# Optimization experiments

Measured on AMD Instinct MI355X. Metric: run time of the kernel, lower is better.

## Reference

```python
import jax, jax.numpy as jnp
import numpy as np

N = 50000          # nodes
E = 800000         # random edges (self-loops added in reference, per PyG default)
B = 64             # graphs in batch
IN_DIM = 773
HID = 256
OUT = 128
H1, D1 = 4, 64     # heads, head_dim layer 1 (256 = 4*64)
H2, D2 = 4, 32     # heads, head_dim layer 2 (128 = 4*32)
NEG_SLOPE = 0.2


def setup_inputs() -> dict:
    key = jax.random.key(0)
    ks = jax.random.split(key, 20)
    s = 0.02
    x = jax.random.normal(ks[0], (N, IN_DIM), dtype=jnp.float32)
    edge_index = jax.random.randint(ks[1], (2, E), 0, N, dtype=jnp.int32)
    batch = jnp.sort(jax.random.randint(ks[2], (N,), 0, B, dtype=jnp.int32))
    return {
        "x": x,
        "edge_index": edge_index,
        "batch": batch,
        "W_in": jax.random.normal(ks[3], (IN_DIM, HID), jnp.float32) * s,
        "b_in": jnp.zeros((HID,), jnp.float32),
        "W1": jax.random.normal(ks[4], (HID, H1 * D1), jnp.float32) * s,
        "att_src1": jax.random.normal(ks[5], (H1, D1), jnp.float32) * s,
        "att_dst1": jax.random.normal(ks[6], (H1, D1), jnp.float32) * s,
        "b1": jnp.zeros((H1 * D1,), jnp.float32),
        "W2": jax.random.normal(ks[7], (HID, H2 * D2), jnp.float32) * s,
        "att_src2": jax.random.normal(ks[8], (H2, D2), jnp.float32) * s,
        "att_dst2": jax.random.normal(ks[9], (H2, D2), jnp.float32) * s,
        "b2": jnp.zeros((H2 * D2,), jnp.float32),
        "W_cls": jax.random.normal(ks[10], (OUT, 2), jnp.float32) * s,
        "b_cls": jnp.zeros((2,), jnp.float32),
        "W_conf": jax.random.normal(ks[11], (OUT, 1), jnp.float32) * s,
        "b_conf": jnp.zeros((1,), jnp.float32),
    }


def _gat_layer(h, src, dst, W, att_src, att_dst, bias, heads, dim):
    # h: (N, F_in). PyG GATConv, concat=True, eval mode (dropout off).
    hW = (h @ W).reshape(N, heads, dim)                    # (N, H, D)
    a_src = jnp.einsum("nhd,hd->nh", hW, att_src)          # (N, H)
    a_dst = jnp.einsum("nhd,hd->nh", hW, att_dst)
    e = a_src[src] + a_dst[dst]                            # (E', H)
    e = jax.nn.leaky_relu(e, NEG_SLOPE)
    # segment softmax over incoming edges of each dst node
    m = jax.ops.segment_max(e, dst, num_segments=N)        # (N, H)
    ex = jnp.exp(e - m[dst])
    z = jax.ops.segment_sum(ex, dst, num_segments=N)       # (N, H)
    alpha = ex / (z[dst] + 1e-16)                          # (E', H)
    msg = hW[src] * alpha[:, :, None]                      # (E', H, D)
    out = jax.ops.segment_sum(msg, dst, num_segments=N)    # (N, H, D)
    return out.reshape(N, heads * dim) + bias


def reference(x, edge_index, batch, W_in, b_in,
              W1, att_src1, att_dst1, b1,
              W2, att_src2, att_dst2, b2,
              W_cls, b_cls, W_conf, b_conf):
    loops = jnp.arange(N, dtype=edge_index.dtype)
    src = jnp.concatenate([edge_index[0], loops])
    dst = jnp.concatenate([edge_index[1], loops])

    h = jax.nn.relu(x @ W_in + b_in)                       # (N, 256)
    h = jax.nn.relu(_gat_layer(h, src, dst, W1, att_src1, att_dst1, b1, H1, D1))
    h = _gat_layer(h, src, dst, W2, att_src2, att_dst2, b2, H2, D2)
    h = jax.nn.relu(h)                                     # (N, 128)

    # global mean pool over graphs
    sums = jax.ops.segment_sum(h, batch, num_segments=B)   # (B, 128)
    cnts = jax.ops.segment_sum(jnp.ones((N,), h.dtype), batch, num_segments=B)
    graph_emb = sums / jnp.maximum(cnts, 1.0)[:, None]

    class_logits = graph_emb @ W_cls + b_cls               # (B, 2)
    confidence = jax.nn.sigmoid(graph_emb @ W_conf + b_conf)  # (B, 1)
    return class_logits, confidence
```

## Files before the change

kernel.cpp:

```cpp
#include <hip/hip_runtime.h>
#include <math.h>

#define NN 50000
#define NE 800000
#define NB 64
#define IND 773
#define MPAD 50048
#define SCAN_B 196

typedef __attribute__((ext_vector_type(8))) short short8_t;
typedef __attribute__((ext_vector_type(4))) float f32x4;

__device__ __forceinline__ float lrelu(float x) { return x > 0.f ? x : 0.2f * x; }
__device__ __forceinline__ short f2b(float f) {
    unsigned u = __float_as_uint(f);
    unsigned r = (u + 0x7fffu + ((u >> 16) & 1u)) >> 16;
    return (short)r;
}
__device__ __forceinline__ float b2f(short s) {
    return __uint_as_float(((unsigned)(unsigned short)s) << 16);
}

#define GLOAD16(g, l) __builtin_amdgcn_global_load_lds(                         \
    (const __attribute__((address_space(1))) void*)(g),                         \
    (__attribute__((address_space(3))) void*)(l), 16, 0, 0)

__global__ __launch_bounds__(512) void gemm_a(const float* __restrict__ X,
                                              const short* __restrict__ Bt,
                                              const float* __restrict__ bias,
                                              short* __restrict__ C) {
    const int K = 800, N = 256;
    __shared__ short As[128 * 32];
    __shared__ short Bs[256 * 32];
    const int t = threadIdx.x;
    const int w = t >> 6, l = t & 63;
    const int l15 = l & 15, lh = l >> 4;
    const int bm = blockIdx.x * 128;
    const int wr = (w >> 2) * 64, wc = (w & 3) * 64;

    const short* bG = Bt + (size_t)(t >> 2) * K + (t & 3) * 8;
    short* bLu = Bs + w * 512;

    f32x4 acc[4][4];
#pragma unroll
    for (int i = 0; i < 4; ++i)
#pragma unroll
        for (int j = 0; j < 4; ++j) acc[i][j] = (f32x4){0.f, 0.f, 0.f, 0.f};

    for (int k0 = 0; k0 < K; k0 += 32) {
        __syncthreads();
        GLOAD16(bG + k0, bLu);
        GLOAD16(bG + (size_t)128 * K + k0, bLu + 128 * 32);
#pragma unroll
        for (int i = 0; i < 4; ++i) {
            int fid = i * 512 + t;
            int row = fid >> 4;
            int cp = fid & 15;
            int gm = bm + row;
            int gk = k0 + cp * 2;
            const float* xp = X + (size_t)gm * IND + gk;
            bool rowok = (gm < NN);
            float v0 = (rowok && gk < IND) ? xp[0] : 0.f;
            float v1 = (rowok && gk + 1 < IND) ? xp[1] : 0.f;
            unsigned pk = ((unsigned)(unsigned short)f2b(v0)) |
                          (((unsigned)(unsigned short)f2b(v1)) << 16);
            *(unsigned*)&As[row * 32 + cp * 2] = pk;
        }
        __syncthreads();
        short8_t af[4], bfr[4];
#pragma unroll
        for (int mi = 0; mi < 4; ++mi)
            af[mi] = *(const short8_t*)&As[(wr + mi * 16 + l15) * 32 + lh * 8];
#pragma unroll
        for (int ni = 0; ni < 4; ++ni)
            bfr[ni] = *(const short8_t*)&Bs[(wc + ni * 16 + l15) * 32 + lh * 8];
#pragma unroll
        for (int mi = 0; mi < 4; ++mi)
#pragma unroll
            for (int ni = 0; ni < 4; ++ni)
                acc[mi][ni] = __builtin_amdgcn_mfma_f32_16x16x32_bf16(af[mi], bfr[ni], acc[mi][ni], 0, 0, 0);
    }
#pragma unroll
    for (int mi = 0; mi < 4; ++mi) {
#pragma unroll
        for (int r = 0; r < 4; ++r) {
            int grow = bm + wr + mi * 16 + lh * 4 + r;
            if (grow >= NN) continue;
#pragma unroll
            for (int ni = 0; ni < 4; ++ni) {
                int gcol = wc + ni * 16 + l15;
                float v = fmaxf(acc[mi][ni][r] + bias[gcol], 0.f);
                C[(size_t)grow * N + gcol] = f2b(v);
            }
        }
    }
}

__global__ __launch_bounds__(512) void gemm_b(const short* __restrict__ A,
                                              const short* __restrict__ Bt,
                                              const float* __restrict__ att_s,
                                              const float* __restrict__ att_d,
                                              short* __restrict__ C,
                                              float* __restrict__ a_s,
                                              float* __restrict__ a_d) {
    const int K = 256, N = 256;
    __shared__ short As[128 * 32];
    __shared__ short Bs[256 * 32];
    const int t = threadIdx.x;
    const int w = t >> 6, l = t & 63;
    const int l15 = l & 15, lh = l >> 4;
    const int bm = blockIdx.x * 128;
    const int wr = (w >> 2) * 64, wc = (w & 3) * 64;

    const short* aG = A + (size_t)(bm + (t >> 2)) * K + (t & 3) * 8;
    const short* bG = Bt + (size_t)(t >> 2) * K + (t & 3) * 8;
    short* aLu = As + w * 512;
    short* bLu = Bs + w * 512;

    f32x4 acc[4][4];
#pragma unroll
    for (int i = 0; i < 4; ++i)
#pragma unroll
        for (int j = 0; j < 4; ++j) acc[i][j] = (f32x4){0.f, 0.f, 0.f, 0.f};

    for (int k0 = 0; k0 < K; k0 += 32) {
        __syncthreads();
        GLOAD16(aG + k0, aLu);
        GLOAD16(bG + k0, bLu);
        GLOAD16(bG + (size_t)128 * K + k0, bLu + 128 * 32);
        __syncthreads();
        short8_t af[4], bfr[4];
#pragma unroll
        for (int mi = 0; mi < 4; ++mi)
            af[mi] = *(const short8_t*)&As[(wr + mi * 16 + l15) * 32 + lh * 8];
#pragma unroll
        for (int ni = 0; ni < 4; ++ni)
            bfr[ni] = *(const short8_t*)&Bs[(wc + ni * 16 + l15) * 32 + lh * 8];
#pragma unroll
        for (int mi = 0; mi < 4; ++mi)
#pragma unroll
            for (int ni = 0; ni < 4; ++ni)
                acc[mi][ni] = __builtin_amdgcn_mfma_f32_16x16x32_bf16(af[mi], bfr[ni], acc[mi][ni], 0, 0, 0);
    }
    const int head = wc >> 6;
    float sa[4], sd[4];
#pragma unroll
    for (int ni = 0; ni < 4; ++ni) {
        sa[ni] = att_s[head * 64 + ni * 16 + l15];
        sd[ni] = att_d[head * 64 + ni * 16 + l15];
    }
#pragma unroll
    for (int mi = 0; mi < 4; ++mi) {
#pragma unroll
        for (int r = 0; r < 4; ++r) {
            int grow = bm + wr + mi * 16 + lh * 4 + r;
            float s = acc[mi][0][r] * sa[0] + acc[mi][1][r] * sa[1] +
                      acc[mi][2][r] * sa[2] + acc[mi][3][r] * sa[3];
            float d = acc[mi][0][r] * sd[0] + acc[mi][1][r] * sd[1] +
                      acc[mi][2][r] * sd[2] + acc[mi][3][r] * sd[3];
#pragma unroll
            for (int off = 1; off < 16; off <<= 1) {
                s += __shfl_xor(s, off);
                d += __shfl_xor(d, off);
            }
            if (grow < NN) {
                if (l15 == 0) { a_s[grow * 4 + head] = s; a_d[grow * 4 + head] = d; }
#pragma unroll
                for (int ni = 0; ni < 4; ++ni)
                    C[(size_t)grow * N + wc + ni * 16 + l15] = f2b(acc[mi][ni][r]);
            }
        }
    }
}

__global__ __launch_bounds__(256) void gemm_c(const short* __restrict__ A,
                                              const short* __restrict__ Bt,
                                              const float* __restrict__ att_s,
                                              const float* __restrict__ att_d,
                                              short* __restrict__ C,
                                              float* __restrict__ a_s,
                                              float* __restrict__ a_d) {
    const int K = 256, N = 128;
    __shared__ short As[128 * 32];
    __shared__ short Bs[128 * 32];
    const int t = threadIdx.x;
    const int w = t >> 6, l = t & 63;
    const int l15 = l & 15, lh = l >> 4;
    const int bm = blockIdx.x * 128;
    const int wr = (w >> 1) * 64, wc = (w & 1) * 64;

    const short* aG = A + (size_t)(bm + w * 32 + (l >> 2)) * K + (l & 3) * 8;
    const short* bG = Bt + (size_t)(w * 32 + (l >> 2)) * K + (l & 3) * 8;
    short* aL = As + (w * 32) * 32;
    short* bL = Bs + (w * 32) * 32;

    f32x4 acc[4][4];
#pragma unroll
    for (int i = 0; i < 4; ++i)
#pragma unroll
        for (int j = 0; j < 4; ++j) acc[i][j] = (f32x4){0.f, 0.f, 0.f, 0.f};

    for (int k0 = 0; k0 < K; k0 += 32) {
        __syncthreads();
        GLOAD16(aG + k0, aL);
        GLOAD16(aG + (size_t)16 * K + k0, aL + 16 * 32);
        GLOAD16(bG + k0, bL);
        GLOAD16(bG + (size_t)16 * K + k0, bL + 16 * 32);
        __syncthreads();
        short8_t af[4], bfr[4];
#pragma unroll
        for (int mi = 0; mi < 4; ++mi)
            af[mi] = *(const short8_t*)&As[(wr + mi * 16 + l15) * 32 + lh * 8];
#pragma unroll
        for (int ni = 0; ni < 4; ++ni)
            bfr[ni] = *(const short8_t*)&Bs[(wc + ni * 16 + l15) * 32 + lh * 8];
#pragma unroll
        for (int mi = 0; mi < 4; ++mi)
#pragma unroll
            for (int ni = 0; ni < 4; ++ni)
                acc[mi][ni] = __builtin_amdgcn_mfma_f32_16x16x32_bf16(af[mi], bfr[ni], acc[mi][ni], 0, 0, 0);
    }
    const int h0 = wc >> 5;
    float sa[4], sd[4];
#pragma unroll
    for (int ni = 0; ni < 4; ++ni) {
        int idx = (h0 + (ni >> 1)) * 32 + (ni & 1) * 16 + l15;
        sa[ni] = att_s[idx];
        sd[ni] = att_d[idx];
    }
#pragma unroll
    for (int mi = 0; mi < 4; ++mi) {
#pragma unroll
        for (int r = 0; r < 4; ++r) {
            int grow = bm + wr + mi * 16 + lh * 4 + r;
            float s0 = acc[mi][0][r] * sa[0] + acc[mi][1][r] * sa[1];
            float s1 = acc[mi][2][r] * sa[2] + acc[mi][3][r] * sa[3];
            float d0 = acc[mi][0][r] * sd[0] + acc[mi][1][r] * sd[1];
            float d1 = acc[mi][2][r] * sd[2] + acc[mi][3][r] * sd[3];
#pragma unroll
            for (int off = 1; off < 16; off <<= 1) {
                s0 += __shfl_xor(s0, off); s1 += __shfl_xor(s1, off);
                d0 += __shfl_xor(d0, off); d1 += __shfl_xor(d1, off);
            }
            if (grow < NN) {
                if (l15 == 0) {
                    a_s[grow * 4 + h0] = s0; a_s[grow * 4 + h0 + 1] = s1;
                    a_d[grow * 4 + h0] = d0; a_d[grow * 4 + h0 + 1] = d1;
                }
#pragma unroll
                for (int ni = 0; ni < 4; ++ni)
                    C[(size_t)grow * N + wc + ni * 16 + l15] = f2b(acc[mi][ni][r]);
            }
        }
    }
}

__global__ __launch_bounds__(256) void k_wt_t(const float* __restrict__ W,
                                              short* __restrict__ Wt,
                                              int K, int N, int Kp) {
    __shared__ short tile[32][33];
    int kb = blockIdx.x * 32, nb = blockIdx.y * 32;
    int tx = threadIdx.x & 31, ty = threadIdx.x >> 5;
#pragma unroll
    for (int r = 0; r < 32; r += 8) {
        int k = kb + ty + r;
        tile[ty + r][tx] = (k < K) ? f2b(W[(size_t)k * N + nb + tx]) : (short)0;
    }
    __syncthreads();
#pragma unroll
    for (int r = 0; r < 32; r += 8) {
        int n = nb + ty + r, k = kb + tx;
        Wt[(size_t)n * Kp + k] = tile[tx][ty + r];
    }
}

__global__ __launch_bounds__(256) void k_zero(int* __restrict__ p, int n) {
    int i = blockIdx.x * 256 + threadIdx.x;
    if (i < n) p[i] = 0;
}

__global__ void k_hist(const int* __restrict__ ei, int* __restrict__ deg) {
    int e = blockIdx.x * 256 + threadIdx.x;
    if (e >= NE) return;
    atomicAdd(&deg[ei[NE + e]], 1);
}

__global__ __launch_bounds__(256) void k_bsum(const int* __restrict__ deg,
                                              int* __restrict__ bsum) {
    int i = blockIdx.x * 256 + threadIdx.x;
    int v = (i < NN) ? deg[i] : 0;
#pragma unroll
    for (int off = 32; off; off >>= 1) v += __shfl_down(v, off);
    __shared__ int ws[4];
    if ((threadIdx.x & 63) == 0) ws[threadIdx.x >> 6] = v;
    __syncthreads();
    if (threadIdx.x == 0) bsum[blockIdx.x] = ws[0] + ws[1] + ws[2] + ws[3];
}

__global__ __launch_bounds__(256) void k_bscan(const int* __restrict__ bsum,
                                               int* __restrict__ boff) {
    int t = threadIdx.x;
    int orig = (t < SCAN_B) ? bsum[t] : 0;
    int v = orig;
    int lane = t & 63, wid = t >> 6;
#pragma unroll
    for (int off = 1; off < 64; off <<= 1) {
        int u = __shfl_up(v, off);
        if (lane >= off) v += u;
    }
    __shared__ int ws[4];
    if (lane == 63) ws[wid] = v;
    __syncthreads();
    int add = 0;
    for (int wq = 0; wq < wid; ++wq) add += ws[wq];
    if (t < SCAN_B) boff[t] = v + add - orig;
}

__global__ __launch_bounds__(256) void k_scan3(const int* __restrict__ deg,
                                               const int* __restrict__ boff,
                                               int* __restrict__ rowp,
                                               int* __restrict__ cursor) {
    int b = blockIdx.x;
    int i = b * 256 + threadIdx.x;
    int d = (i < NN) ? deg[i] : 0;
    int v = d;
    int lane = threadIdx.x & 63, wid = threadIdx.x >> 6;
#pragma unroll
    for (int off = 1; off < 64; off <<= 1) {
        int u = __shfl_up(v, off);
        if (lane >= off) v += u;
    }
    __shared__ int ws[4];
    if (lane == 63) ws[wid] = v;
    __syncthreads();
    int add = boff[b];
    for (int wq = 0; wq < wid; ++wq) add += ws[wq];
    int excl = add + v - d;
    if (i < NN) { rowp[i] = excl; cursor[i] = excl; }
    if (i == NN - 1) rowp[NN] = excl + d;
}

__global__ void k_scatter(const int* __restrict__ ei, int* __restrict__ cursor,
                          int* __restrict__ colidx) {
    int e = blockIdx.x * 256 + threadIdx.x;
    if (e >= NE) return;
    int s = ei[e], d = ei[NE + e];
    int pos = atomicAdd(&cursor[d], 1);
    colidx[pos] = s;
}

template<int HD>
__global__ __launch_bounds__(256) void gat_agg(const short* __restrict__ hW,
                                               const float* __restrict__ a_s,
                                               const float* __restrict__ a_d,
                                               const int* __restrict__ row_ptr,
                                               const int* __restrict__ colidx,
                                               const float* __restrict__ bias,
                                               short* __restrict__ outp) {
    const int CPL = HD / 64;
    int node = blockIdx.x * 4 + (threadIdx.x >> 6);
    int lane = threadIdx.x & 63;
    if (node >= NN) return;
    int h = lane >> 4;
    int start = row_ptr[node], end = row_ptr[node + 1];
    float adst = a_d[node * 4 + h];
    float eself = lrelu(a_s[node * 4 + h] + adst);

    float z = 1.f;
    float acc[CPL];
    {
        const short* row = hW + (size_t)node * HD + lane * CPL;
        if (CPL == 4) { short4 q = *(const short4*)row; acc[0]=b2f(q.x); acc[1]=b2f(q.y); acc[2]=b2f(q.z); acc[3]=b2f(q.w); }
        else          { short2 q = *(const short2*)row; acc[0]=b2f(q.x); acc[1]=b2f(q.y); }
    }
    for (int e = start; e < end; e += 8) {
        int sidx[8];
        float xs[8], ex[8];
#pragma unroll
        for (int q = 0; q < 8; ++q) {
            int ee = e + q;
            sidx[q] = colidx[ee < end ? ee : end - 1];
        }
#pragma unroll
        for (int q = 0; q < 8; ++q) xs[q] = a_s[sidx[q] * 4 + h];
        float v[8][CPL];
        if (CPL == 4) {
#pragma unroll
            for (int q = 0; q < 8; ++q) {
                short4 qq = *(const short4*)(hW + (size_t)sidx[q] * HD + lane * 4);
                v[q][0]=b2f(qq.x); v[q][1]=b2f(qq.y); v[q][2]=b2f(qq.z); v[q][3]=b2f(qq.w);
            }
        } else {
#pragma unroll
            for (int q = 0; q < 8; ++q) {
                short2 qq = *(const short2*)(hW + (size_t)sidx[q] * HD + lane * 2);
                v[q][0]=b2f(qq.x); v[q][1]=b2f(qq.y);
            }
        }
#pragma unroll
        for (int q = 0; q < 8; ++q) {
            float w = __expf(lrelu(xs[q] + adst) - eself);
            ex[q] = (e + q < end) ? w : 0.f;
        }
#pragma unroll
        for (int q = 0; q < 8; ++q) z += ex[q];
#pragma unroll
        for (int j = 0; j < CPL; ++j) {
            float a = 0.f;
#pragma unroll
            for (int q = 0; q < 8; ++q) a += ex[q] * v[q][j];
            acc[j] += a;
        }
    }
    float inv = 1.f / z;
    short* orow = outp + (size_t)node * HD + lane * CPL;
#pragma unroll
    for (int j = 0; j < CPL; ++j)
        orow[j] = f2b(fmaxf(acc[j] * inv + bias[lane * CPL + j], 0.f));
}

__global__ __launch_bounds__(512) void pool_head(const short* __restrict__ h2,
                                                 const int* __restrict__ batch,
                                                 const float* __restrict__ W_cls,
                                                 const float* __restrict__ b_cls,
                                                 const float* __restrict__ W_conf,
                                                 const float* __restrict__ b_conf,
                                                 float* __restrict__ out) {
    int b = blockIdx.x;
    int t = threadIdx.x & 127;
    int g = threadIdx.x >> 7;
    int lo = 0, hi = NN;
    while (lo < hi) { int mid = (lo + hi) >> 1; if (batch[mid] < b) lo = mid + 1; else hi = mid; }
    int start = lo;
    lo = 0; hi = NN;
    while (lo < hi) { int mid = (lo + hi) >> 1; if (batch[mid] < b + 1) lo = mid + 1; else hi = mid; }
    int end = lo;

    float acc = 0.f;
    for (int n = start + g; n < end; n += 4) acc += b2f(h2[(size_t)n * 128 + t]);
    __shared__ float se[4][128];
    se[g][t] = acc;
    __syncthreads();
    if (g == 0) {
        float emb = (se[0][t] + se[1][t] + se[2][t] + se[3][t]) /
                    fmaxf((float)(end - start), 1.f);
        se[0][t] = emb;
    }
    __syncthreads();
    if (threadIdx.x == 0) {
        float v = b_cls[0];
        for (int c = 0; c < 128; ++c) v += se[0][c] * W_cls[c * 2 + 0];
        out[b * 2 + 0] = v;
    } else if (threadIdx.x == 1) {
        float v = b_cls[1];
        for (int c = 0; c < 128; ++c) v += se[0][c] * W_cls[c * 2 + 1];
        out[b * 2 + 1] = v;
    } else if (threadIdx.x == 2) {
        float v = b_conf[0];
        for (int c = 0; c < 128; ++c) v += se[0][c] * W_conf[c];
        out[128 + b] = 1.f / (1.f + expf(-v));
    }
}

extern "C" void kernel_launch(void* const* d_in, const int* in_sizes, int n_in,
                              void* d_out, int out_size, void* d_ws, size_t ws_size,
                              hipStream_t stream) {
    const float* x        = (const float*)d_in[0];
    const int*   ei       = (const int*)d_in[1];
    const int*   batch    = (const int*)d_in[2];
    const float* W_in     = (const float*)d_in[3];
    const float* b_in     = (const float*)d_in[4];
    const float* W1       = (const float*)d_in[5];
    const float* att_src1 = (const float*)d_in[6];
    const float* att_dst1 = (const float*)d_in[7];
    const float* b1       = (const float*)d_in[8];
    const float* W2       = (const float*)d_in[9];
    const float* att_src2 = (const float*)d_in[10];
    const float* att_dst2 = (const float*)d_in[11];
    const float* b2       = (const float*)d_in[12];
    const float* W_cls    = (const float*)d_in[13];
    const float* b_cls    = (const float*)d_in[14];
    const float* W_conf   = (const float*)d_in[15];
    const float* b_conf   = (const float*)d_in[16];
    float* out = (float*)d_out;

    char* ws = (char*)d_ws;
    short* h0  = (short*)(ws + 0);
    short* hW1 = (short*)(ws + 25624576);
    short* h1  = (short*)(ws + 51249152);
    short* hW2 = (short*)(ws + 76873728);
    short* h2  = (short*)(ws + 89686016);
    size_t base = 102498304;
    short* Wt_in = (short*)(ws + base);
    short* Wt1   = (short*)(ws + base + 409600);
    short* Wt2   = (short*)(ws + base + 540672);
    float* a_s1  = (float*)(ws + base + 606208);
    float* a_d1  = (float*)(ws + base + 1406208);
    int*   deg    = (int*)(ws + base + 2206208);
    int*   rowp   = (int*)(ws + base + 2406208);
    int*   cursor = (int*)(ws + base + 2606272);
    int*   colidx = (int*)(ws + base + 2806272);
    int*   bsum   = (int*)(ws + base + 6006272);
    int*   boff   = (int*)(ws + base + 6007296);

    k_wt_t<<<dim3(25, 8), 256, 0, stream>>>(W_in, Wt_in, IND, 256, 800);
    k_wt_t<<<dim3(8, 8), 256, 0, stream>>>(W1, Wt1, 256, 256, 256);
    k_wt_t<<<dim3(8, 4), 256, 0, stream>>>(W2, Wt2, 256, 128, 256);

    k_zero<<<SCAN_B, 256, 0, stream>>>(deg, NN);
    k_hist<<<NE / 256, 256, 0, stream>>>(ei, deg);
    k_bsum<<<SCAN_B, 256, 0, stream>>>(deg, bsum);
    k_bscan<<<1, 256, 0, stream>>>(bsum, boff);
    k_scan3<<<SCAN_B, 256, 0, stream>>>(deg, boff, rowp, cursor);
    k_scatter<<<NE / 256, 256, 0, stream>>>(ei, cursor, colidx);

    gemm_a<<<391, 512, 0, stream>>>(x, Wt_in, b_in, h0);
    gemm_b<<<391, 512, 0, stream>>>(h0, Wt1, att_src1, att_dst1, hW1, a_s1, a_d1);
    gat_agg<256><<<12500, 256, 0, stream>>>(hW1, a_s1, a_d1, rowp, colidx, b1, h1);
    gemm_c<<<391, 256, 0, stream>>>(h1, Wt2, att_src2, att_dst2, hW2, a_s1, a_d1);
    gat_agg<128><<<12500, 256, 0, stream>>>(hW2, a_s1, a_d1, rowp, colidx, b2, h2);
    pool_head<<<NB, 512, 0, stream>>>(h2, batch, W_cls, b_cls, W_conf, b_conf, out);
}
```

Measured before the change: 409.3 us.

## Double-buffer input GEMM with register prefetch and split layer-1 GEMM over columns

The first GEMM now keeps two LDS buffers. It prefetches the next X tile into registers, using vectorized float4 loads converted to bf16, while MFMAs run on the current tile, so each k-step needs one barrier instead of two. The layer-1 GEMM switches from 512-thread blocks covering all 256 columns to 256-thread blocks over a 2D grid of 128-column tiles. That doubles the block count, which should improve occupancy and wave balance. The costs are extra LDS use, more register pressure in gemm_a, and A tiles being re-read once per column tile in gemm_b.

```diff
diff --git a/kernel.cpp b/kernel.cpp
--- a/kernel.cpp
+++ b/kernel.cpp
@@ -29,17 +29,19 @@
                                               const short* __restrict__ Bt,
                                               const float* __restrict__ bias,
                                               short* __restrict__ C) {
-    const int K = 800, N = 256;
-    __shared__ short As[128 * 32];
-    __shared__ short Bs[256 * 32];
+    const int K = 800, N = 256, NT = 25;
+    __shared__ short As[2][128 * 32];
+    __shared__ short Bs[2][256 * 32];
     const int t = threadIdx.x;
     const int w = t >> 6, l = t & 63;
     const int l15 = l & 15, lh = l >> 4;
     const int bm = blockIdx.x * 128;
     const int wr = (w >> 2) * 64, wc = (w & 3) * 64;
-
+    const int arow = t >> 2, acb = (t & 3) * 8;
+    const int gm = bm + arow;
+    const bool rowok = gm < NN;
+    const float* xrow = X + (size_t)gm * IND;
     const short* bG = Bt + (size_t)(t >> 2) * K + (t & 3) * 8;
-    short* bLu = Bs + w * 512;
 
     f32x4 acc[4][4];
 #pragma unroll
@@ -47,39 +49,53 @@
 #pragma unroll
         for (int j = 0; j < 4; ++j) acc[i][j] = (f32x4){0.f, 0.f, 0.f, 0.f};
 
-    for (int k0 = 0; k0 < K; k0 += 32) {
-        __syncthreads();
-        GLOAD16(bG + k0, bLu);
-        GLOAD16(bG + (size_t)128 * K + k0, bLu + 128 * 32);
-#pragma unroll
-        for (int i = 0; i < 4; ++i) {
-            int fid = i * 512 + t;
-            int row = fid >> 4;
-            int cp = fid & 15;
-            int gm = bm + row;
-            int gk = k0 + cp * 2;
-            const float* xp = X + (size_t)gm * IND + gk;
-            bool rowok = (gm < NN);
-            float v0 = (rowok && gk < IND) ? xp[0] : 0.f;
-            float v1 = (rowok && gk + 1 < IND) ? xp[1] : 0.f;
-            unsigned pk = ((unsigned)(unsigned short)f2b(v0)) |
-                          (((unsigned)(unsigned short)f2b(v1)) << 16);
-            *(unsigned*)&As[row * 32 + cp * 2] = pk;
-        }
-        __syncthreads();
+    short8_t rA;
+    auto loadA = [&](int it) {
+        int gk = it * 32 + acb;
+        if (rowok && gk + 7 < IND) {
+            float4 v0 = *(const float4*)(xrow + gk);
+            float4 v1 = *(const float4*)(xrow + gk + 4);
+            rA[0] = f2b(v0.x); rA[1] = f2b(v0.y); rA[2] = f2b(v0.z); rA[3] = f2b(v0.w);
+            rA[4] = f2b(v1.x); rA[5] = f2b(v1.y); rA[6] = f2b(v1.z); rA[7] = f2b(v1.w);
+        } else {
+#pragma unroll
+            for (int j = 0; j < 8; ++j)
+                rA[j] = (rowok && gk + j < IND) ? f2b(xrow[gk + j]) : (short)0;
+        }
+    };
+
+    loadA(0);
+    GLOAD16(bG, &Bs[0][w * 512]);
+    GLOAD16(bG + (size_t)128 * K, &Bs[0][128 * 32 + w * 512]);
+    *(short8_t*)&As[0][arow * 32 + acb] = rA;
+    loadA(1);
+    GLOAD16(bG + 32, &Bs[1][w * 512]);
+    GLOAD16(bG + (size_t)128 * K + 32, &Bs[1][128 * 32 + w * 512]);
+    __syncthreads();
+
+    for (int it = 0; it < NT; ++it) {
+        const int c = it & 1, n = c ^ 1;
         short8_t af[4], bfr[4];
 #pragma unroll
         for (int mi = 0; mi < 4; ++mi)
-            af[mi] = *(const short8_t*)&As[(wr + mi * 16 + l15) * 32 + lh * 8];
+            af[mi] = *(const short8_t*)&As[c][(wr + mi * 16 + l15) * 32 + lh * 8];
 #pragma unroll
         for (int ni = 0; ni < 4; ++ni)
-            bfr[ni] = *(const short8_t*)&Bs[(wc + ni * 16 + l15) * 32 + lh * 8];
+            bfr[ni] = *(const short8_t*)&Bs[c][(wc + ni * 16 + l15) * 32 + lh * 8];
+        if (it + 1 < NT) *(short8_t*)&As[n][arow * 32 + acb] = rA;
+        if (it + 2 < NT) loadA(it + 2);
 #pragma unroll
         for (int mi = 0; mi < 4; ++mi)
 #pragma unroll
             for (int ni = 0; ni < 4; ++ni)
                 acc[mi][ni] = __builtin_amdgcn_mfma_f32_16x16x32_bf16(af[mi], bfr[ni], acc[mi][ni], 0, 0, 0);
-    }
+        __syncthreads();
+        if (it + 2 < NT) {
+            GLOAD16(bG + (it + 2) * 32, &Bs[c][w * 512]);
+            GLOAD16(bG + (size_t)128 * K + (it + 2) * 32, &Bs[c][128 * 32 + w * 512]);
+        }
+    }
+
 #pragma unroll
     for (int mi = 0; mi < 4; ++mi) {
 #pragma unroll
@@ -96,7 +112,7 @@
     }
 }
 
-__global__ __launch_bounds__(512) void gemm_b(const short* __restrict__ A,
+__global__ __launch_bounds__(256) void gemm_b(const short* __restrict__ A,
                                               const short* __restrict__ Bt,
                                               const float* __restrict__ att_s,
                                               const float* __restrict__ att_d,
@@ -105,17 +121,17 @@
                                               float* __restrict__ a_d) {
     const int K = 256, N = 256;
     __shared__ short As[128 * 32];
-    __shared__ short Bs[256 * 32];
+    __shared__ short Bs[128 * 32];
     const int t = threadIdx.x;
     const int w = t >> 6, l = t & 63;
     const int l15 = l & 15, lh = l >> 4;
-    const int bm = blockIdx.x * 128;
-    const int wr = (w >> 2) * 64, wc = (w & 3) * 64;
-
-    const short* aG = A + (size_t)(bm + (t >> 2)) * K + (t & 3) * 8;
-    const short* bG = Bt + (size_t)(t >> 2) * K + (t & 3) * 8;
-    short* aLu = As + w * 512;
-    short* bLu = Bs + w * 512;
+    const int bm = blockIdx.x * 128, bn = blockIdx.y * 128;
+    const int wr = (w >> 1) * 64, wc = (w & 1) * 64;
+
+    const short* aG = A + (size_t)(bm + w * 32 + (l >> 2)) * K + (l & 3) * 8;
+    const short* bG = Bt + (size_t)(bn + w * 32 + (l >> 2)) * K + (l & 3) * 8;
+    short* aL = As + (w * 32) * 32;
+    short* bL = Bs + (w * 32) * 32;
 
     f32x4 acc[4][4];
 #pragma unroll
@@ -125,9 +141,10 @@
 
     for (int k0 = 0; k0 < K; k0 += 32) {
         __syncthreads();
-        GLOAD16(aG + k0, aLu);
-        GLOAD16(bG + k0, bLu);
-        GLOAD16(bG + (size_t)128 * K + k0, bLu + 128 * 32);
+        GLOAD16(aG + k0, aL);
+        GLOAD16(aG + (size_t)16 * K + k0, aL + 16 * 32);
+        GLOAD16(bG + k0, bL);
+        GLOAD16(bG + (size_t)16 * K + k0, bL + 16 * 32);
         __syncthreads();
         short8_t af[4], bfr[4];
 #pragma unroll
@@ -142,7 +159,7 @@
             for (int ni = 0; ni < 4; ++ni)
                 acc[mi][ni] = __builtin_amdgcn_mfma_f32_16x16x32_bf16(af[mi], bfr[ni], acc[mi][ni], 0, 0, 0);
     }
-    const int head = wc >> 6;
+    const int head = (bn + wc) >> 6;
     float sa[4], sd[4];
 #pragma unroll
     for (int ni = 0; ni < 4; ++ni) {
@@ -167,7 +184,7 @@
                 if (l15 == 0) { a_s[grow * 4 + head] = s; a_d[grow * 4 + head] = d; }
 #pragma unroll
                 for (int ni = 0; ni < 4; ++ni)
-                    C[(size_t)grow * N + wc + ni * 16 + l15] = f2b(acc[mi][ni][r]);
+                    C[(size_t)grow * N + bn + wc + ni * 16 + l15] = f2b(acc[mi][ni][r]);
             }
         }
     }
@@ -515,7 +532,7 @@
     k_scatter<<<NE / 256, 256, 0, stream>>>(ei, cursor, colidx);
 
     gemm_a<<<391, 512, 0, stream>>>(x, Wt_in, b_in, h0);
-    gemm_b<<<391, 512, 0, stream>>>(h0, Wt1, att_src1, att_dst1, hW1, a_s1, a_d1);
+    gemm_b<<<dim3(391, 2), 256, 0, stream>>>(h0, Wt1, att_src1, att_dst1, hW1, a_s1, a_d1);
     gat_agg<256><<<12500, 256, 0, stream>>>(hW1, a_s1, a_d1, rowp, colidx, b1, h1);
     gemm_c<<<391, 256, 0, stream>>>(h1, Wt2, att_src2, att_dst2, hW2, a_s1, a_d1);
     gat_agg<128><<<12500, 256, 0, stream>>>(hW2, a_s1, a_d1, rowp, colidx, b2, h2);
```

Result: faster. 380.5 us (-7.0%).
